# Kernel tuning notes

Measured on AMD Instinct MI355X. Metric: run time of the kernel, lower is better.

Reference implementation:

```python
import jax, jax.numpy as jnp
import numpy as np

N_HEADS = 16


def setup_inputs() -> dict:
    key = jax.random.key(0)
    ks = jax.random.split(key, 12)
    B, S, D = 2, 2048, 1024
    inp = {
        "query": jax.random.normal(ks[0], (B, S, D), jnp.float32),
        "key": jax.random.normal(ks[1], (B, S, D), jnp.float32),
        "value": jax.random.normal(ks[2], (B, S, D), jnp.float32),
        "mask": jnp.ones((B, S), jnp.int32),
        "Wq": jax.random.normal(ks[3], (D, D), jnp.float32) * 0.02,
        "bq": jax.random.normal(ks[4], (D,), jnp.float32) * 0.02,
        "Wk": jax.random.normal(ks[5], (D, D), jnp.float32) * 0.02,
        "bk": jax.random.normal(ks[6], (D,), jnp.float32) * 0.02,
        "Wv": jax.random.normal(ks[7], (D, D), jnp.float32) * 0.02,
        "bv": jax.random.normal(ks[8], (D,), jnp.float32) * 0.02,
        "Wo": jax.random.normal(ks[9], (D, D), jnp.float32) * 0.02,
        "bo": jax.random.normal(ks[10], (D,), jnp.float32) * 0.02,
    }
    return inp


def _shape(x, bs, n_heads, d_head):
    # (bs, seq, dim) -> (bs, n_heads, seq, d_head)
    return x.reshape(bs, -1, n_heads, d_head).transpose(0, 2, 1, 3)


def reference(query, key, value, mask, Wq, bq, Wk, bk, Wv, bv, Wo, bo):
    bs, q_len, dim = query.shape
    d_head = dim // N_HEADS

    q = _shape(query @ Wq + bq, bs, N_HEADS, d_head) / jnp.sqrt(jnp.asarray(d_head, query.dtype))
    k = _shape(key @ Wk + bk, bs, N_HEADS, d_head)
    v = _shape(value @ Wv + bv, bs, N_HEADS, d_head)

    scores = jnp.einsum("bhqd,bhkd->bhqk", q, k)  # [bs, h, q_len, k_len]
    neg = jnp.finfo(scores.dtype).min
    scores = jnp.where((mask == 0)[:, None, None, :], neg, scores)
    weights = jax.nn.softmax(scores, axis=-1)  # dropout p=0 -> identity

    context = jnp.einsum("bhqk,bhkd->bhqd", weights, v)
    context = context.transpose(0, 2, 1, 3).reshape(bs, q_len, dim)
    return context @ Wo + bo
```

## Files before the change

### kernel.cpp

```cpp
#include <hip/hip_runtime.h>
#include <hip/hip_bf16.h>
#include <stdint.h>

typedef short s16x8 __attribute__((ext_vector_type(8)));
typedef float f32x4 __attribute__((ext_vector_type(4)));
typedef float f32x16 __attribute__((ext_vector_type(16)));

union FragU { uint4 u; s16x8 v; };

static __device__ __forceinline__ uint32_t pk2bf(float a, float b) {
  union { __hip_bfloat162 h; uint32_t u; } cv;
  cv.h = __float22bfloat162_rn(make_float2(a, b));
  return cv.u;
}

static __device__ __forceinline__ unsigned short f2bf(float f) {
  union { float f; uint32_t u; } x; x.f = f;
  uint32_t r = x.u + 0x7FFFu + ((x.u >> 16) & 1u);
  return (unsigned short)(r >> 16);
}

static __device__ __forceinline__ void gl_lds16(const void* g, void* lds_wave_base) {
  __builtin_amdgcn_global_load_lds(
      (const __attribute__((address_space(1))) uint32_t*)(uintptr_t)g,
      (__attribute__((address_space(3))) uint32_t*)(uintptr_t)lds_wave_base, 16, 0, 0);
}

__global__ __launch_bounds__(256) void wt4_kernel(const float* __restrict__ W0,
                                                  const float* __restrict__ W1,
                                                  const float* __restrict__ W2,
                                                  const float* __restrict__ W3,
                                                  unsigned short* __restrict__ T0,
                                                  unsigned short* __restrict__ T1,
                                                  unsigned short* __restrict__ T2,
                                                  unsigned short* __restrict__ T3) {
  __shared__ unsigned short tile[64][68];
  const int z = blockIdx.z;
  const float* W = (z == 0) ? W0 : (z == 1) ? W1 : (z == 2) ? W2 : W3;
  unsigned short* WT = (z == 0) ? T0 : (z == 1) ? T1 : (z == 2) ? T2 : T3;
  const int t = threadIdx.x;
  const int n0 = blockIdx.x * 64, k0 = blockIdx.y * 64;
  const int r = t >> 4, c4 = (t & 15) * 4;
#pragma unroll
  for (int i = 0; i < 4; ++i) {
    const int k = i * 16 + r;
    const float4 v = *(const float4*)&W[(k0 + k) * 1024 + n0 + c4];
    tile[k][c4 + 0] = f2bf(v.x);
    tile[k][c4 + 1] = f2bf(v.y);
    tile[k][c4 + 2] = f2bf(v.z);
    tile[k][c4 + 3] = f2bf(v.w);
  }
  __syncthreads();
#pragma unroll
  for (int i = 0; i < 4; ++i) {
    const int n = i * 16 + r;
    ushort4 o;
    o.x = tile[c4 + 0][n];
    o.y = tile[c4 + 1][n];
    o.z = tile[c4 + 2][n];
    o.w = tile[c4 + 3][n];
    *(ushort4*)&WT[(n0 + n) * 1024 + k0 + c4] = o;
  }
}

__global__ __launch_bounds__(256) void cvt3_kernel(const float* __restrict__ q,
                                                   const float* __restrict__ k,
                                                   const float* __restrict__ v,
                                                   unsigned short* __restrict__ Qc,
                                                   unsigned short* __restrict__ Kc,
                                                   unsigned short* __restrict__ Vc) {
  const int z = blockIdx.x >> 11, blk = blockIdx.x & 2047;
  const float* src = (z == 0) ? q : (z == 1) ? k : v;
  unsigned short* dst = (z == 0) ? Qc : (z == 1) ? Kc : Vc;
  const size_t base = ((size_t)blk * 256 + threadIdx.x) * 8;
  const float4 f0 = *(const float4*)(src + base);
  const float4 f1 = *(const float4*)(src + base + 4);
  const uint4 o{pk2bf(f0.x, f0.y), pk2bf(f0.z, f0.w), pk2bf(f1.x, f1.y), pk2bf(f1.z, f1.w)};
  *(uint4*)(dst + base) = o;
}

__global__ __launch_bounds__(256, 3) void qkv_gemm_bf16(const unsigned short* __restrict__ Aq,
                                                        const unsigned short* __restrict__ Ak,
                                                        const unsigned short* __restrict__ Av,
                                                        const unsigned short* __restrict__ Wq,
                                                        const unsigned short* __restrict__ Wk,
                                                        const unsigned short* __restrict__ Wv,
                                                        const float* __restrict__ bq,
                                                        const float* __restrict__ bk,
                                                        const float* __restrict__ bv,
                                                        unsigned short* __restrict__ Qb,
                                                        unsigned short* __restrict__ Kb,
                                                        unsigned short* __restrict__ Vt,
                                                        const float qscale) {
  __shared__ char AsB[3][8192];
  __shared__ char BsB[3][8192];
  const int t = threadIdx.x;
  const int z = blockIdx.z;
  const unsigned short* A = (z == 0) ? Aq : (z == 1) ? Ak : Av;
  const unsigned short* BT = (z == 0) ? Wq : (z == 1) ? Wk : Wv;
  const float* bias = (z == 0) ? bq : (z == 1) ? bk : bv;
  const float scale = (z == 0) ? qscale : 1.0f;

  const int lane = t & 63, w = t >> 6;
  const int g = lane >> 4, li = lane & 15;
  const int wr = (w >> 1) * 64, wc = (w & 1) * 64;
  const int lin = blockIdx.x + 8 * blockIdx.y;
  const int work = (lin & 7) * 32 + (lin >> 3);
  const int m0 = (work >> 3) * 128, n0 = (work & 7) * 128;

  const int r1 = t >> 2, c1 = (t & 3) ^ ((r1 >> 1) & 3);
  const int r2 = r1 + 64, c2 = (t & 3) ^ ((r2 >> 1) & 3);

  auto stage = [&](int kt, int buf) {
    const int k0 = kt * 32;
    gl_lds16(A + (size_t)(m0 + r1) * 1024 + k0 + c1 * 8, &AsB[buf][0] + (w << 10));
    gl_lds16(A + (size_t)(m0 + r2) * 1024 + k0 + c2 * 8, &AsB[buf][0] + 4096 + (w << 10));
    gl_lds16(BT + (size_t)(n0 + r1) * 1024 + k0 + c1 * 8, &BsB[buf][0] + (w << 10));
    gl_lds16(BT + (size_t)(n0 + r2) * 1024 + k0 + c2 * 8, &BsB[buf][0] + 4096 + (w << 10));
  };

  f32x4 acc[4][4] = {};
  stage(0, 0);
  stage(1, 1);
  asm volatile("s_waitcnt vmcnt(4)" ::: "memory");
  asm volatile("s_barrier" ::: "memory");

  int cur = 0;
  for (int kt = 0; kt < 32; ++kt) {
    if (kt < 30) {
      int nb = cur + 2; if (nb >= 3) nb -= 3;
      stage(kt + 2, nb);
    }
    const char* Ab = &AsB[cur][0];
    const char* Bb = &BsB[cur][0];
    FragU a[4], bf[4];
#pragma unroll
    for (int i = 0; i < 4; ++i) {
      const int ra = wr + i * 16 + li;
      a[i].u = *(const uint4*)(Ab + ra * 64 + ((g ^ ((ra >> 1) & 3)) << 4));
      const int rb = wc + i * 16 + li;
      bf[i].u = *(const uint4*)(Bb + rb * 64 + ((g ^ ((rb >> 1) & 3)) << 4));
    }
#pragma unroll
    for (int fm = 0; fm < 4; ++fm)
#pragma unroll
      for (int fn = 0; fn < 4; ++fn)
        acc[fm][fn] = __builtin_amdgcn_mfma_f32_16x16x32_bf16(a[fm].v, bf[fn].v, acc[fm][fn], 0, 0, 0);

    if (kt < 30) {
      asm volatile("s_waitcnt vmcnt(4)" ::: "memory");
    } else if (kt == 30) {
      asm volatile("s_waitcnt vmcnt(0)" ::: "memory");
    }
    if (kt < 31) asm volatile("s_barrier" ::: "memory");
    cur = (cur == 2) ? 0 : cur + 1;
  }

  unsigned short* OutN = (z == 0) ? Qb : Kb;
#pragma unroll
  for (int fn = 0; fn < 4; ++fn) {
    const int n = n0 + wc + fn * 16 + li;
    const float bv2 = bias[n];
#pragma unroll
    for (int fm = 0; fm < 4; ++fm) {
      const int mb = m0 + wr + fm * 16 + g * 4;
      const f32x4 v = acc[fm][fn];
      ushort4 pk;
      pk.x = f2bf((v[0] + bv2) * scale);
      pk.y = f2bf((v[1] + bv2) * scale);
      pk.z = f2bf((v[2] + bv2) * scale);
      pk.w = f2bf((v[3] + bv2) * scale);
      if (z == 2) {
        const int bb = mb >> 11, s = mb & 2047;
        *(ushort4*)&Vt[(size_t)(bb * 1024 + n) * 2048 + s] = pk;
      } else {
        unsigned short* o = OutN;
        o[(size_t)(mb + 0) * 1024 + n] = pk.x;
        o[(size_t)(mb + 1) * 1024 + n] = pk.y;
        o[(size_t)(mb + 2) * 1024 + n] = pk.z;
        o[(size_t)(mb + 3) * 1024 + n] = pk.w;
      }
    }
  }
}

__global__ __launch_bounds__(256, 3) void qkv_gemm_f32(const float* __restrict__ Aq,
                                                       const float* __restrict__ Ak,
                                                       const float* __restrict__ Av,
                                                       const unsigned short* __restrict__ Wq,
                                                       const unsigned short* __restrict__ Wk,
                                                       const unsigned short* __restrict__ Wv,
                                                       const float* __restrict__ bq,
                                                       const float* __restrict__ bk,
                                                       const float* __restrict__ bv,
                                                       unsigned short* __restrict__ Qb,
                                                       unsigned short* __restrict__ Kb,
                                                       unsigned short* __restrict__ Vt,
                                                       const float qscale) {
  __shared__ unsigned short As[2][128 * 32];
  __shared__ unsigned short Bs[2][128 * 32];
  const int t = threadIdx.x;
  const int z = blockIdx.z;
  const float* A = (z == 0) ? Aq : (z == 1) ? Ak : Av;
  const unsigned short* BT = (z == 0) ? Wq : (z == 1) ? Wk : Wv;
  const float* bias = (z == 0) ? bq : (z == 1) ? bk : bv;
  const float scale = (z == 0) ? qscale : 1.0f;

  const int lane = t & 63, w = t >> 6;
  const int g = lane >> 4, li = lane & 15;
  const int wr = (w >> 1) * 64, wc = (w & 1) * 64;
  const int lin = blockIdx.x + 8 * blockIdx.y;
  const int work = (lin & 7) * 32 + (lin >> 3);
  const int m0 = (work >> 3) * 128, n0 = (work & 7) * 128;

  const int arow = t >> 1, ac0 = (t & 1) * 2, asw = (arow >> 1) & 3;
  const int br1 = t >> 2, bg1 = (t & 3) ^ ((br1 >> 1) & 3);
  const int br2 = br1 + 64, bg2 = (t & 3) ^ ((br2 >> 1) & 3);

  auto stageB = [&](int k0, int buf) {
    gl_lds16(BT + (size_t)(n0 + br1) * 1024 + k0 + bg1 * 8, (char*)&Bs[buf][0] + (w << 10));
    gl_lds16(BT + (size_t)(n0 + br2) * 1024 + k0 + bg2 * 8, (char*)&Bs[buf][0] + 4096 + (w << 10));
  };

  uint4 ar0, ar1;
  auto loadA = [&](int k0) {
    const float* ga = A + (size_t)(m0 + arow) * 1024 + k0 + ac0 * 8;
    const float4 f0 = *(const float4*)(ga + 0), f1 = *(const float4*)(ga + 4);
    const float4 f2 = *(const float4*)(ga + 8), f3 = *(const float4*)(ga + 12);
    ar0 = uint4{pk2bf(f0.x, f0.y), pk2bf(f0.z, f0.w), pk2bf(f1.x, f1.y), pk2bf(f1.z, f1.w)};
    ar1 = uint4{pk2bf(f2.x, f2.y), pk2bf(f2.z, f2.w), pk2bf(f3.x, f3.y), pk2bf(f3.z, f3.w)};
  };
  auto storeA = [&](int buf) {
    char* ab = (char*)&As[buf][0] + arow * 64;
    *(uint4*)(ab + ((ac0 ^ asw) << 4)) = ar0;
    *(uint4*)(ab + (((ac0 + 1) ^ asw) << 4)) = ar1;
  };

  f32x4 acc[4][4] = {};
  stageB(0, 0);
  loadA(0);
  storeA(0);
  __syncthreads();
  int cur = 0;
  for (int k0 = 0; k0 < 1024; k0 += 32) {
    const bool more = (k0 + 32) < 1024;
    if (more) {
      stageB(k0 + 32, cur ^ 1);
      loadA(k0 + 32);
    }
    const char* Ab = (const char*)&As[cur][0];
    const char* Bb = (const char*)&Bs[cur][0];
    FragU a[4], bf[4];
#pragma unroll
    for (int i = 0; i < 4; ++i) {
      const int rowa = wr + i * 16 + li;
      a[i].u = *(const uint4*)(Ab + rowa * 64 + (((g) ^ ((rowa >> 1) & 3)) << 4));
      const int rowb = wc + i * 16 + li;
      bf[i].u = *(const uint4*)(Bb + rowb * 64 + (((g) ^ ((rowb >> 1) & 3)) << 4));
    }
#pragma unroll
    for (int fm = 0; fm < 4; ++fm)
#pragma unroll
      for (int fn = 0; fn < 4; ++fn)
        acc[fm][fn] = __builtin_amdgcn_mfma_f32_16x16x32_bf16(a[fm].v, bf[fn].v, acc[fm][fn], 0, 0, 0);
    if (more) storeA(cur ^ 1);
    __syncthreads();
    cur ^= 1;
  }

  unsigned short* OutN = (z == 0) ? Qb : Kb;
#pragma unroll
  for (int fn = 0; fn < 4; ++fn) {
    const int n = n0 + wc + fn * 16 + li;
    const float bv2 = bias[n];
#pragma unroll
    for (int fm = 0; fm < 4; ++fm) {
      const int mb = m0 + wr + fm * 16 + g * 4;
      const f32x4 v = acc[fm][fn];
      ushort4 pk;
      pk.x = f2bf((v[0] + bv2) * scale);
      pk.y = f2bf((v[1] + bv2) * scale);
      pk.z = f2bf((v[2] + bv2) * scale);
      pk.w = f2bf((v[3] + bv2) * scale);
      if (z == 2) {
        const int bb = mb >> 11, s = mb & 2047;
        *(ushort4*)&Vt[(size_t)(bb * 1024 + n) * 2048 + s] = pk;
      } else {
        unsigned short* o = OutN;
        o[(size_t)(mb + 0) * 1024 + n] = pk.x;
        o[(size_t)(mb + 1) * 1024 + n] = pk.y;
        o[(size_t)(mb + 2) * 1024 + n] = pk.z;
        o[(size_t)(mb + 3) * 1024 + n] = pk.w;
      }
    }
  }
}

__global__ __launch_bounds__(256, 3) void out_gemm(const unsigned short* __restrict__ A,
                                                   const unsigned short* __restrict__ BT,
                                                   const float* __restrict__ bias,
                                                   float* __restrict__ Out) {
  __shared__ char AsB[3][8192];
  __shared__ char BsB[3][8192];
  const int t = threadIdx.x;
  const int lane = t & 63, w = t >> 6;
  const int g = lane >> 4, li = lane & 15;
  const int wr = (w >> 1) * 64, wc = (w & 1) * 64;
  const int lin = blockIdx.x + 8 * blockIdx.y;
  const int work = (lin & 7) * 32 + (lin >> 3);
  const int m0 = (work >> 3) * 128, n0 = (work & 7) * 128;

  const int r1 = t >> 2, c1 = (t & 3) ^ ((r1 >> 1) & 3);
  const int r2 = r1 + 64, c2 = (t & 3) ^ ((r2 >> 1) & 3);

  auto stage = [&](int kt, int buf) {
    const int k0 = kt * 32;
    gl_lds16(A + (size_t)(m0 + r1) * 1024 + k0 + c1 * 8, &AsB[buf][0] + (w << 10));
    gl_lds16(A + (size_t)(m0 + r2) * 1024 + k0 + c2 * 8, &AsB[buf][0] + 4096 + (w << 10));
    gl_lds16(BT + (size_t)(n0 + r1) * 1024 + k0 + c1 * 8, &BsB[buf][0] + (w << 10));
    gl_lds16(BT + (size_t)(n0 + r2) * 1024 + k0 + c2 * 8, &BsB[buf][0] + 4096 + (w << 10));
  };

  f32x4 acc[4][4] = {};
  stage(0, 0);
  stage(1, 1);
  asm volatile("s_waitcnt vmcnt(4)" ::: "memory");
  asm volatile("s_barrier" ::: "memory");

  int cur = 0;
  for (int kt = 0; kt < 32; ++kt) {
    if (kt < 30) {
      int nb = cur + 2; if (nb >= 3) nb -= 3;
      stage(kt + 2, nb);
    }
    const char* Ab = &AsB[cur][0];
    const char* Bb = &BsB[cur][0];
    FragU a[4], bf[4];
#pragma unroll
    for (int i = 0; i < 4; ++i) {
      const int ra = wr + i * 16 + li;
      a[i].u = *(const uint4*)(Ab + ra * 64 + ((g ^ ((ra >> 1) & 3)) << 4));
      const int rb = wc + i * 16 + li;
      bf[i].u = *(const uint4*)(Bb + rb * 64 + ((g ^ ((rb >> 1) & 3)) << 4));
    }
#pragma unroll
    for (int fm = 0; fm < 4; ++fm)
#pragma unroll
      for (int fn = 0; fn < 4; ++fn)
        acc[fm][fn] = __builtin_amdgcn_mfma_f32_16x16x32_bf16(a[fm].v, bf[fn].v, acc[fm][fn], 0, 0, 0);

    if (kt < 30) {
      asm volatile("s_waitcnt vmcnt(4)" ::: "memory");
    } else if (kt == 30) {
      asm volatile("s_waitcnt vmcnt(0)" ::: "memory");
    }
    if (kt < 31) asm volatile("s_barrier" ::: "memory");
    cur = (cur == 2) ? 0 : cur + 1;
  }

#pragma unroll
  for (int fn = 0; fn < 4; ++fn) {
    const int n = n0 + wc + fn * 16 + li;
    const float bv = bias[n];
#pragma unroll
    for (int fm = 0; fm < 4; ++fm) {
      const int mb = m0 + wr + fm * 16 + g * 4;
      const f32x4 v = acc[fm][fn];
#pragma unroll
      for (int r = 0; r < 4; ++r) Out[(size_t)(mb + r) * 1024 + n] = v[r] + bv;
    }
  }
}

__global__ __launch_bounds__(256, 2) void attn_kernel(const unsigned short* __restrict__ Qb,
                                                      const unsigned short* __restrict__ Kb,
                                                      const unsigned short* __restrict__ Vt,
                                                      const int* __restrict__ mask,
                                                      unsigned short* __restrict__ ctx) {
  __shared__ unsigned short Ks[2][64 * 64];
  __shared__ unsigned short Vs[2][64 * 64];
  const int t = threadIdx.x, lane = t & 63, w = t >> 6;
  const int l31 = lane & 31, hi = lane >> 5;
  const int d0 = blockIdx.x + 16 * blockIdx.y;
  const int work = (d0 & 7) * 64 + (d0 >> 3);
  const int qblk = work & 15, bh = work >> 4;
  const int b = bh >> 4, h = bh & 15;
  const int q0 = qblk * 128;
  const int qrow = b * 2048 + q0 + w * 32 + l31;

  const int srow = t >> 3, sch = t & 7;

  uint4 kr0, kr1, vr0, vr1;
  int mv = 1;
  auto loadKV = [&](int kvn) {
    const unsigned short* kbase = Kb + (size_t)(b * 2048 + kvn) * 1024 + h * 64;
    kr0 = *(const uint4*)(kbase + (size_t)srow * 1024 + sch * 8);
    kr1 = *(const uint4*)(kbase + (size_t)(srow + 32) * 1024 + sch * 8);
    const unsigned short* vbase = Vt + (size_t)(b * 1024 + h * 64) * 2048 + kvn;
    vr0 = *(const uint4*)(vbase + (size_t)srow * 2048 + sch * 8);
    vr1 = *(const uint4*)(vbase + (size_t)(srow + 32) * 2048 + sch * 8);
    mv = mask[b * 2048 + kvn + lane];
  };
  auto storeKV = [&](int buf) {
    char* kb = (char*)&Ks[buf][0];
    char* vb = (char*)&Vs[buf][0];
    const int o0 = srow * 128 + ((sch * 16) ^ ((srow & 7) << 4));
    const int o1 = (srow + 32) * 128 + ((sch * 16) ^ ((srow & 7) << 4));
    *(uint4*)(kb + o0) = kr0;
    *(uint4*)(kb + o1) = kr1;
    *(uint4*)(vb + o0) = vr0;
    *(uint4*)(vb + o1) = vr1;
  };

  FragU qf[4];
  {
    const unsigned short* qb = Qb + (size_t)qrow * 1024 + h * 64 + hi * 8;
#pragma unroll
    for (int dc = 0; dc < 4; ++dc) qf[dc].u = *(const uint4*)(qb + dc * 16);
  }

  loadKV(0);
  storeKV(0);
  __syncthreads();

  f32x16 acc[2] = {};
  float m_run = 8.0f, l_run = 0.f;
  int cur = 0;

  for (int tile = 0; tile < 32; ++tile) {
    const bool more = tile + 1 < 32;
    const int mvcur = mv;
    if (more) loadKV((tile + 1) * 64);

    f32x16 sc[2] = {};
    {
      const char* kb = (const char*)&Ks[cur][0];
      __builtin_amdgcn_s_setprio(1);
#pragma unroll
      for (int t2 = 0; t2 < 2; ++t2) {
        const int row = t2 * 32 + l31;
        const int sw = (row & 7) << 4;
        const int rb = row * 128;
#pragma unroll
        for (int dc = 0; dc < 4; ++dc) {
          FragU kf;
          kf.u = *(const uint4*)(kb + rb + ((16 * (dc * 2 + hi)) ^ sw));
          sc[t2] = __builtin_amdgcn_mfma_f32_32x32x16_bf16(kf.v, qf[dc].v, sc[t2], 0, 0, 0);
        }
      }
      __builtin_amdgcn_s_setprio(0);
    }

    if (!__all(mvcur != 0)) {
#pragma unroll
      for (int t2 = 0; t2 < 2; ++t2)
#pragma unroll
        for (int r = 0; r < 16; ++r) {
          const int kvv = t2 * 32 + (r & 3) + 8 * (r >> 2) + 4 * hi;
          sc[t2][r] += (__shfl(mvcur, kvv, 64) ? 0.f : -30000.f);
        }
    }

    float pm = sc[0][0];
#pragma unroll
    for (int t2 = 0; t2 < 2; ++t2)
#pragma unroll
      for (int r = 0; r < 16; ++r) pm = fmaxf(pm, sc[t2][r]);
    pm = fmaxf(pm, __shfl_xor(pm, 32, 64));

    if (!__all(pm <= m_run + 8.f)) {
      const float m_new = fmaxf(m_run, pm);
      const float rsc = __builtin_amdgcn_exp2f(m_run - m_new);
      m_run = m_new;
      l_run *= rsc;
#pragma unroll
      for (int dt = 0; dt < 2; ++dt)
#pragma unroll
        for (int r = 0; r < 16; ++r) acc[dt][r] *= rsc;
    }

    float rs = 0.f;
#pragma unroll
    for (int t2 = 0; t2 < 2; ++t2)
#pragma unroll
      for (int r = 0; r < 16; ++r) {
        const float e = __builtin_amdgcn_exp2f(sc[t2][r] - m_run);
        sc[t2][r] = e;
        rs += e;
      }
    l_run += rs;

    FragU pf[4];
#pragma unroll
    for (int ks = 0; ks < 4; ++ks) {
      const int t2 = ks >> 1, s8 = (ks & 1) * 8;
      uint32_t U = pk2bf(sc[t2][s8 + 0], sc[t2][s8 + 1]);
      uint32_t V2 = pk2bf(sc[t2][s8 + 2], sc[t2][s8 + 3]);
      uint32_t X = pk2bf(sc[t2][s8 + 4], sc[t2][s8 + 5]);
      uint32_t Y = pk2bf(sc[t2][s8 + 6], sc[t2][s8 + 7]);
      asm("v_permlane32_swap_b32 %0, %1" : "+v"(U), "+v"(X));
      asm("v_permlane32_swap_b32 %0, %1" : "+v"(V2), "+v"(Y));
      pf[ks].u = uint4{U, V2, X, Y};
    }

    {
      const char* vb = (const char*)&Vs[cur][0];
      __builtin_amdgcn_s_setprio(1);
#pragma unroll
      for (int dt = 0; dt < 2; ++dt) {
        const int drow = dt * 32 + l31;
        const int sw = (drow & 7) << 4;
        const int rb = drow * 128;
#pragma unroll
        for (int ks = 0; ks < 4; ++ks) {
          FragU vf;
          vf.u = *(const uint4*)(vb + rb + ((16 * (ks * 2 + hi)) ^ sw));
          acc[dt] = __builtin_amdgcn_mfma_f32_32x32x16_bf16(vf.v, pf[ks].v, acc[dt], 0, 0, 0);
        }
      }
      __builtin_amdgcn_s_setprio(0);
    }

    if (more) storeKV(cur ^ 1);
    __syncthreads();
    cur ^= 1;
  }

  const float l_tot = l_run + __shfl_xor(l_run, 32, 64);
  const float inv_l = 1.0f / l_tot;
  unsigned short* cb = ctx + (size_t)qrow * 1024 + h * 64;
#pragma unroll
  for (int dt = 0; dt < 2; ++dt)
#pragma unroll
    for (int rq = 0; rq < 4; ++rq) {
      uint2 o;
      o.x = pk2bf(acc[dt][rq * 4 + 0] * inv_l, acc[dt][rq * 4 + 1] * inv_l);
      o.y = pk2bf(acc[dt][rq * 4 + 2] * inv_l, acc[dt][rq * 4 + 3] * inv_l);
      *(uint2*)(cb + dt * 32 + rq * 8 + hi * 4) = o;
    }
}

extern "C" void kernel_launch(void* const* d_in, const int* in_sizes, int n_in,
                              void* d_out, int out_size, void* d_ws, size_t ws_size,
                              hipStream_t stream) {
  const float* query = (const float*)d_in[0];
  const float* key = (const float*)d_in[1];
  const float* value = (const float*)d_in[2];
  const int* mask = (const int*)d_in[3];
  const float* Wq = (const float*)d_in[4];
  const float* bq = (const float*)d_in[5];
  const float* Wk = (const float*)d_in[6];
  const float* bk = (const float*)d_in[7];
  const float* Wv = (const float*)d_in[8];
  const float* bv = (const float*)d_in[9];
  const float* Wo = (const float*)d_in[10];
  const float* bo = (const float*)d_in[11];
  float* out = (float*)d_out;

  const size_t MB = 1024 * 1024;
  if (ws_size < 40 * MB) return;
  char* ws = (char*)d_ws;
  unsigned short* WqT = (unsigned short*)(ws);
  unsigned short* WkT = (unsigned short*)(ws + 2 * MB);
  unsigned short* WvT = (unsigned short*)(ws + 4 * MB);
  unsigned short* WoT = (unsigned short*)(ws + 6 * MB);
  unsigned short* Qb = (unsigned short*)(ws + 8 * MB);
  unsigned short* Kb = (unsigned short*)(ws + 16 * MB);
  unsigned short* Vt = (unsigned short*)(ws + 24 * MB);
  unsigned short* ctx = (unsigned short*)(ws + 32 * MB);

  const dim3 tb(256);
  wt4_kernel<<<dim3(16, 16, 4), tb, 0, stream>>>(Wq, Wk, Wv, Wo, WqT, WkT, WvT, WoT);

  const float qscale = 0.125f * 1.4426950408889634f;

  if (ws_size >= 64 * MB) {
    unsigned short* Qc = (unsigned short*)(ws + 40 * MB);
    unsigned short* Kc = (unsigned short*)(ws + 48 * MB);
    unsigned short* Vc = (unsigned short*)(ws + 56 * MB);
    cvt3_kernel<<<dim3(6144), tb, 0, stream>>>(query, key, value, Qc, Kc, Vc);
    qkv_gemm_bf16<<<dim3(8, 32, 3), tb, 0, stream>>>(Qc, Kc, Vc, WqT, WkT, WvT,
                                                     bq, bk, bv, Qb, Kb, Vt, qscale);
  } else {
    qkv_gemm_f32<<<dim3(8, 32, 3), tb, 0, stream>>>(query, key, value, WqT, WkT, WvT,
                                                    bq, bk, bv, Qb, Kb, Vt, qscale);
  }

  attn_kernel<<<dim3(16, 32), tb, 0, stream>>>(Qb, Kb, Vt, mask, ctx);

  out_gemm<<<dim3(8, 32), tb, 0, stream>>>(ctx, WoT, bo, out);
}
```

Baseline: 121.5 us.

## Split KV range across wave pairs in attention and merge prep kernels

The attention kernel now uses 64-query blocks with two wave pairs. Each pair processes alternating 64-key tiles (even and odd), so the grid doubles to 1024 blocks and occupancy rises to 4 blocks per CU. Partial softmax states are merged through LDS at the end. K and V loads are split and staged at different points in the loop to overlap with compute. The weight transpose and the input bf16 conversion are fused into one prep launch to remove a kernel launch. The costs are an extra reduction, more barriers, and more register pressure under the tighter launch bound.

```diff
diff --git a/kernel.cpp b/kernel.cpp
--- a/kernel.cpp
+++ b/kernel.cpp
@@ -24,6 +24,62 @@
   __builtin_amdgcn_global_load_lds(
       (const __attribute__((address_space(1))) uint32_t*)(uintptr_t)g,
       (__attribute__((address_space(3))) uint32_t*)(uintptr_t)lds_wave_base, 16, 0, 0);
+}
+
+__global__ __launch_bounds__(256) void prep_kernel(const float* __restrict__ W0,
+                                                   const float* __restrict__ W1,
+                                                   const float* __restrict__ W2,
+                                                   const float* __restrict__ W3,
+                                                   unsigned short* __restrict__ T0,
+                                                   unsigned short* __restrict__ T1,
+                                                   unsigned short* __restrict__ T2,
+                                                   unsigned short* __restrict__ T3,
+                                                   const float* __restrict__ qs,
+                                                   const float* __restrict__ ks,
+                                                   const float* __restrict__ vs,
+                                                   unsigned short* __restrict__ Qc,
+                                                   unsigned short* __restrict__ Kc,
+                                                   unsigned short* __restrict__ Vc) {
+  __shared__ unsigned short tile[64][68];
+  const int blk = blockIdx.x;
+  const int t = threadIdx.x;
+  if (blk < 1024) {
+    const int z = blk >> 8;
+    const float* W = (z == 0) ? W0 : (z == 1) ? W1 : (z == 2) ? W2 : W3;
+    unsigned short* WT = (z == 0) ? T0 : (z == 1) ? T1 : (z == 2) ? T2 : T3;
+    const int n0 = (blk & 15) * 64, k0 = ((blk >> 4) & 15) * 64;
+    const int r = t >> 4, c4 = (t & 15) * 4;
+#pragma unroll
+    for (int i = 0; i < 4; ++i) {
+      const int k = i * 16 + r;
+      const float4 v = *(const float4*)&W[(k0 + k) * 1024 + n0 + c4];
+      tile[k][c4 + 0] = f2bf(v.x);
+      tile[k][c4 + 1] = f2bf(v.y);
+      tile[k][c4 + 2] = f2bf(v.z);
+      tile[k][c4 + 3] = f2bf(v.w);
+    }
+    __syncthreads();
+#pragma unroll
+    for (int i = 0; i < 4; ++i) {
+      const int n = i * 16 + r;
+      ushort4 o;
+      o.x = tile[c4 + 0][n];
+      o.y = tile[c4 + 1][n];
+      o.z = tile[c4 + 2][n];
+      o.w = tile[c4 + 3][n];
+      *(ushort4*)&WT[(n0 + n) * 1024 + k0 + c4] = o;
+    }
+  } else {
+    const int c = blk - 1024;
+    const int z = c >> 11, sub = c & 2047;
+    const float* src = (z == 0) ? qs : (z == 1) ? ks : vs;
+    unsigned short* dst = (z == 0) ? Qc : (z == 1) ? Kc : Vc;
+    const size_t base = ((size_t)sub * 256 + t) * 8;
+    const float4 f0 = *(const float4*)(src + base);
+    const float4 f1 = *(const float4*)(src + base + 4);
+    const uint4 o{pk2bf(f0.x, f0.y), pk2bf(f0.z, f0.w), pk2bf(f1.x, f1.y), pk2bf(f1.z, f1.w)};
+    *(uint4*)(dst + base) = o;
+  }
 }
 
 __global__ __launch_bounds__(256) void wt4_kernel(const float* __restrict__ W0,
@@ -61,22 +117,6 @@
     o.w = tile[c4 + 3][n];
     *(ushort4*)&WT[(n0 + n) * 1024 + k0 + c4] = o;
   }
-}
-
-__global__ __launch_bounds__(256) void cvt3_kernel(const float* __restrict__ q,
-                                                   const float* __restrict__ k,
-                                                   const float* __restrict__ v,
-                                                   unsigned short* __restrict__ Qc,
-                                                   unsigned short* __restrict__ Kc,
-                                                   unsigned short* __restrict__ Vc) {
-  const int z = blockIdx.x >> 11, blk = blockIdx.x & 2047;
-  const float* src = (z == 0) ? q : (z == 1) ? k : v;
-  unsigned short* dst = (z == 0) ? Qc : (z == 1) ? Kc : Vc;
-  const size_t base = ((size_t)blk * 256 + threadIdx.x) * 8;
-  const float4 f0 = *(const float4*)(src + base);
-  const float4 f1 = *(const float4*)(src + base + 4);
-  const uint4 o{pk2bf(f0.x, f0.y), pk2bf(f0.z, f0.w), pk2bf(f1.x, f1.y), pk2bf(f1.z, f1.w)};
-  *(uint4*)(dst + base) = o;
 }
 
 __global__ __launch_bounds__(256, 3) void qkv_gemm_bf16(const unsigned short* __restrict__ Aq,
@@ -372,44 +412,54 @@
   }
 }
 
-__global__ __launch_bounds__(256, 2) void attn_kernel(const unsigned short* __restrict__ Qb,
+__global__ __launch_bounds__(256, 4) void attn_kernel(const unsigned short* __restrict__ Qb,
                                                       const unsigned short* __restrict__ Kb,
                                                       const unsigned short* __restrict__ Vt,
                                                       const int* __restrict__ mask,
                                                       unsigned short* __restrict__ ctx) {
-  __shared__ unsigned short Ks[2][64 * 64];
-  __shared__ unsigned short Vs[2][64 * 64];
+  __shared__ char smem[32768];
   const int t = threadIdx.x, lane = t & 63, w = t >> 6;
   const int l31 = lane & 31, hi = lane >> 5;
-  const int d0 = blockIdx.x + 16 * blockIdx.y;
-  const int work = (d0 & 7) * 64 + (d0 >> 3);
-  const int qblk = work & 15, bh = work >> 4;
+  const int p = w & 1;
+  const int d0 = blockIdx.x;
+  const int work = (d0 & 7) * 128 + (d0 >> 3);
+  const int qblk = work & 31, bh = work >> 5;
   const int b = bh >> 4, h = bh & 15;
-  const int q0 = qblk * 128;
-  const int qrow = b * 2048 + q0 + w * 32 + l31;
+  const int qrow = b * 2048 + qblk * 64 + (w >> 1) * 32 + l31;
 
   const int srow = t >> 3, sch = t & 7;
-
-  uint4 kr0, kr1, vr0, vr1;
-  int mv = 1;
-  auto loadKV = [&](int kvn) {
-    const unsigned short* kbase = Kb + (size_t)(b * 2048 + kvn) * 1024 + h * 64;
-    kr0 = *(const uint4*)(kbase + (size_t)srow * 1024 + sch * 8);
-    kr1 = *(const uint4*)(kbase + (size_t)(srow + 32) * 1024 + sch * 8);
-    const unsigned short* vbase = Vt + (size_t)(b * 1024 + h * 64) * 2048 + kvn;
-    vr0 = *(const uint4*)(vbase + (size_t)srow * 2048 + sch * 8);
-    vr1 = *(const uint4*)(vbase + (size_t)(srow + 32) * 2048 + sch * 8);
-    mv = mask[b * 2048 + kvn + lane];
-  };
-  auto storeKV = [&](int buf) {
-    char* kb = (char*)&Ks[buf][0];
-    char* vb = (char*)&Vs[buf][0];
+  char* Ksp = smem + p * 8192;
+  char* Vsp = smem + 16384 + p * 8192;
+
+  const unsigned short* Kbase = Kb + (size_t)(b * 2048) * 1024 + h * 64;
+  const unsigned short* Vbase = Vt + (size_t)(b * 1024 + h * 64) * 2048;
+
+  uint4 kre0, kre1, kro0, kro1, vre0, vre1, vro0, vro1;
+  int mv_next;
+  auto loadK = [&](int i) {
+    const int ke = (2 * i) * 64, ko = ke + 64;
+    kre0 = *(const uint4*)(Kbase + (size_t)(ke + srow) * 1024 + sch * 8);
+    kre1 = *(const uint4*)(Kbase + (size_t)(ke + srow + 32) * 1024 + sch * 8);
+    kro0 = *(const uint4*)(Kbase + (size_t)(ko + srow) * 1024 + sch * 8);
+    kro1 = *(const uint4*)(Kbase + (size_t)(ko + srow + 32) * 1024 + sch * 8);
+    mv_next = mask[b * 2048 + (2 * i + p) * 64 + lane];
+  };
+  auto loadV = [&](int i) {
+    const int ke = (2 * i) * 64, ko = ke + 64;
+    vre0 = *(const uint4*)(Vbase + (size_t)srow * 2048 + ke + sch * 8);
+    vre1 = *(const uint4*)(Vbase + (size_t)(srow + 32) * 2048 + ke + sch * 8);
+    vro0 = *(const uint4*)(Vbase + (size_t)srow * 2048 + ko + sch * 8);
+    vro1 = *(const uint4*)(Vbase + (size_t)(srow + 32) * 2048 + ko + sch * 8);
+  };
+  auto storeKV = [&]() {
     const int o0 = srow * 128 + ((sch * 16) ^ ((srow & 7) << 4));
     const int o1 = (srow + 32) * 128 + ((sch * 16) ^ ((srow & 7) << 4));
-    *(uint4*)(kb + o0) = kr0;
-    *(uint4*)(kb + o1) = kr1;
-    *(uint4*)(vb + o0) = vr0;
-    *(uint4*)(vb + o1) = vr1;
+    char* k0 = smem;          char* k1 = smem + 8192;
+    char* v0 = smem + 16384;  char* v1 = smem + 24576;
+    *(uint4*)(k0 + o0) = kre0; *(uint4*)(k0 + o1) = kre1;
+    *(uint4*)(k1 + o0) = kro0; *(uint4*)(k1 + o1) = kro1;
+    *(uint4*)(v0 + o0) = vre0; *(uint4*)(v0 + o1) = vre1;
+    *(uint4*)(v1 + o0) = vro0; *(uint4*)(v1 + o1) = vro1;
   };
 
   FragU qf[4];
@@ -419,22 +469,22 @@
     for (int dc = 0; dc < 4; ++dc) qf[dc].u = *(const uint4*)(qb + dc * 16);
   }
 
-  loadKV(0);
-  storeKV(0);
-  __syncthreads();
+  loadK(0);
+  loadV(0);
+  storeKV();
+  int mv_cur = mv_next;
+  asm volatile("s_waitcnt lgkmcnt(0)" ::: "memory");
+  __builtin_amdgcn_s_barrier();
+  loadK(1);
 
   f32x16 acc[2] = {};
   float m_run = 8.0f, l_run = 0.f;
-  int cur = 0;
-
-  for (int tile = 0; tile < 32; ++tile) {
-    const bool more = tile + 1 < 32;
-    const int mvcur = mv;
-    if (more) loadKV((tile + 1) * 64);
+
+  for (int i = 0; i < 16; ++i) {
+    const int mvcur = mv_cur;
 
     f32x16 sc[2] = {};
     {
-      const char* kb = (const char*)&Ks[cur][0];
       __builtin_amdgcn_s_setprio(1);
 #pragma unroll
       for (int t2 = 0; t2 < 2; ++t2) {
@@ -444,7 +494,7 @@
 #pragma unroll
         for (int dc = 0; dc < 4; ++dc) {
           FragU kf;
-          kf.u = *(const uint4*)(kb + rb + ((16 * (dc * 2 + hi)) ^ sw));
+          kf.u = *(const uint4*)(Ksp + rb + ((16 * (dc * 2 + hi)) ^ sw));
           sc[t2] = __builtin_amdgcn_mfma_f32_32x32x16_bf16(kf.v, qf[dc].v, sc[t2], 0, 0, 0);
         }
       }
@@ -478,6 +528,8 @@
 #pragma unroll
         for (int r = 0; r < 16; ++r) acc[dt][r] *= rsc;
     }
+
+    if (i < 15) loadV(i + 1);
 
     float rs = 0.f;
 #pragma unroll
@@ -504,7 +556,6 @@
     }
 
     {
-      const char* vb = (const char*)&Vs[cur][0];
       __builtin_amdgcn_s_setprio(1);
 #pragma unroll
       for (int dt = 0; dt < 2; ++dt) {
@@ -514,30 +565,59 @@
 #pragma unroll
         for (int ks = 0; ks < 4; ++ks) {
           FragU vf;
-          vf.u = *(const uint4*)(vb + rb + ((16 * (ks * 2 + hi)) ^ sw));
+          vf.u = *(const uint4*)(Vsp + rb + ((16 * (ks * 2 + hi)) ^ sw));
           acc[dt] = __builtin_amdgcn_mfma_f32_32x32x16_bf16(vf.v, pf[ks].v, acc[dt], 0, 0, 0);
         }
       }
       __builtin_amdgcn_s_setprio(0);
     }
 
-    if (more) storeKV(cur ^ 1);
-    __syncthreads();
-    cur ^= 1;
-  }
-
-  const float l_tot = l_run + __shfl_xor(l_run, 32, 64);
-  const float inv_l = 1.0f / l_tot;
-  unsigned short* cb = ctx + (size_t)qrow * 1024 + h * 64;
-#pragma unroll
-  for (int dt = 0; dt < 2; ++dt)
-#pragma unroll
-    for (int rq = 0; rq < 4; ++rq) {
-      uint2 o;
-      o.x = pk2bf(acc[dt][rq * 4 + 0] * inv_l, acc[dt][rq * 4 + 1] * inv_l);
-      o.y = pk2bf(acc[dt][rq * 4 + 2] * inv_l, acc[dt][rq * 4 + 3] * inv_l);
-      *(uint2*)(cb + dt * 32 + rq * 8 + hi * 4) = o;
-    }
+    if (i < 15) {
+      __builtin_amdgcn_s_barrier();
+      storeKV();
+      mv_cur = mv_next;
+      asm volatile("s_waitcnt lgkmcnt(0)" ::: "memory");
+      __builtin_amdgcn_s_barrier();
+      if (i < 14) loadK(i + 2);
+    }
+  }
+
+  __builtin_amdgcn_s_barrier();
+  float* exch = (float*)smem;
+  float* myex = exch + (w >> 1) * (64 * 37) + lane * 37;
+  if (p) {
+    const float l_red = l_run + __shfl_xor(l_run, 32, 64);
+#pragma unroll
+    for (int dt = 0; dt < 2; ++dt)
+#pragma unroll
+      for (int r = 0; r < 16; ++r) myex[dt * 16 + r] = acc[dt][r];
+    myex[32] = m_run;
+    myex[33] = l_red;
+  }
+  asm volatile("s_waitcnt lgkmcnt(0)" ::: "memory");
+  __builtin_amdgcn_s_barrier();
+  if (!p) {
+    const float m_b = myex[32], l_b = myex[33];
+    const float l_a = l_run + __shfl_xor(l_run, 32, 64);
+    const float m = fmaxf(m_run, m_b);
+    const float ea = __builtin_amdgcn_exp2f(m_run - m);
+    const float eb = __builtin_amdgcn_exp2f(m_b - m);
+    const float inv_l = 1.0f / (l_a * ea + l_b * eb);
+    unsigned short* cb = ctx + (size_t)qrow * 1024 + h * 64;
+#pragma unroll
+    for (int dt = 0; dt < 2; ++dt)
+#pragma unroll
+      for (int rq = 0; rq < 4; ++rq) {
+        float v0 = (acc[dt][rq * 4 + 0] * ea + myex[dt * 16 + rq * 4 + 0] * eb) * inv_l;
+        float v1 = (acc[dt][rq * 4 + 1] * ea + myex[dt * 16 + rq * 4 + 1] * eb) * inv_l;
+        float v2 = (acc[dt][rq * 4 + 2] * ea + myex[dt * 16 + rq * 4 + 2] * eb) * inv_l;
+        float v3 = (acc[dt][rq * 4 + 3] * ea + myex[dt * 16 + rq * 4 + 3] * eb) * inv_l;
+        uint2 o;
+        o.x = pk2bf(v0, v1);
+        o.y = pk2bf(v2, v3);
+        *(uint2*)(cb + dt * 32 + rq * 8 + hi * 4) = o;
+      }
+  }
 }
 
 extern "C" void kernel_launch(void* const* d_in, const int* in_sizes, int n_in,
@@ -570,23 +650,23 @@
   unsigned short* ctx = (unsigned short*)(ws + 32 * MB);
 
   const dim3 tb(256);
-  wt4_kernel<<<dim3(16, 16, 4), tb, 0, stream>>>(Wq, Wk, Wv, Wo, WqT, WkT, WvT, WoT);
-
   const float qscale = 0.125f * 1.4426950408889634f;
 
   if (ws_size >= 64 * MB) {
     unsigned short* Qc = (unsigned short*)(ws + 40 * MB);
     unsigned short* Kc = (unsigned short*)(ws + 48 * MB);
     unsigned short* Vc = (unsigned short*)(ws + 56 * MB);
-    cvt3_kernel<<<dim3(6144), tb, 0, stream>>>(query, key, value, Qc, Kc, Vc);
+    prep_kernel<<<dim3(7168), tb, 0, stream>>>(Wq, Wk, Wv, Wo, WqT, WkT, WvT, WoT,
+                                               query, key, value, Qc, Kc, Vc);
     qkv_gemm_bf16<<<dim3(8, 32, 3), tb, 0, stream>>>(Qc, Kc, Vc, WqT, WkT, WvT,
                                                      bq, bk, bv, Qb, Kb, Vt, qscale);
   } else {
+    wt4_kernel<<<dim3(16, 16, 4), tb, 0, stream>>>(Wq, Wk, Wv, Wo, WqT, WkT, WvT, WoT);
     qkv_gemm_f32<<<dim3(8, 32, 3), tb, 0, stream>>>(query, key, value, WqT, WkT, WvT,
                                                     bq, bk, bv, Qb, Kb, Vt, qscale);
   }
 
-  attn_kernel<<<dim3(16, 32), tb, 0, stream>>>(Qb, Kb, Vt, mask, ctx);
+  attn_kernel<<<dim3(1024), tb, 0, stream>>>(Qb, Kb, Vt, mask, ctx);
 
   out_gemm<<<dim3(8, 32), tb, 0, stream>>>(ctx, WoT, bo, out);
 }
```

Measured after the change: 225.2 us. 85.3% more time.
